# Kernel tuning notes

Measured on AMD Instinct MI355X. Metric: run time of the kernel, lower is better.

Reference implementation:

```python
import jax, jax.numpy as jnp
import numpy as np

H = 8  # num_heads, fixed in the module


def setup_inputs() -> dict:
    key = jax.random.key(0)
    ks = jax.random.split(key, 26)
    C = 256          # hidden_dim
    K = 16           # num_corners
    B = 8            # images
    P = 64           # proposals per image
    N = B * P        # total proposals
    Hf = Wf = 14     # feature map HxW (T = 196 keys per proposal)
    Hq = Wq = 10     # query grid (S = 100 queries)
    s = 1.0 / np.sqrt(C)

    def w(k, shape):
        return jax.random.normal(k, shape, jnp.float32) * s

    return {
        "features": jax.random.normal(ks[0], (N, C, Hf, Wf), jnp.float32),
        "query_features": jax.random.normal(ks[1], (B, C, Hq, Wq), jnp.float32),
        # self-attention params (torch MHA: y = x @ W.T + b)
        "wq_s": w(ks[2], (C, C)), "wk_s": w(ks[3], (C, C)), "wv_s": w(ks[4], (C, C)),
        "bq_s": jnp.zeros((C,), jnp.float32), "bk_s": jnp.zeros((C,), jnp.float32), "bv_s": jnp.zeros((C,), jnp.float32),
        "wo_s": w(ks[5], (C, C)), "bo_s": jnp.zeros((C,), jnp.float32),
        # cross-attention params
        "wq_c": w(ks[6], (C, C)), "wk_c": w(ks[7], (C, C)), "wv_c": w(ks[8], (C, C)),
        "bq_c": jnp.zeros((C,), jnp.float32), "bk_c": jnp.zeros((C,), jnp.float32), "bv_c": jnp.zeros((C,), jnp.float32),
        "wo_c": w(ks[9], (C, C)), "bo_c": jnp.zeros((C,), jnp.float32),
        # polygon MLP head
        "w1": w(ks[10], (C, C)), "b1": jnp.zeros((C,), jnp.float32),
        "w2": w(ks[11], (2 * K, C)), "b2": jnp.zeros((2 * K,), jnp.float32),
        # score head
        "ws": w(ks[12], (1, C)), "bs": jnp.zeros((1,), jnp.float32),
    }


def _forward(features, query_features,
             wq_s, wk_s, wv_s, bq_s, bk_s, bv_s, wo_s, bo_s,
             wq_c, wk_c, wv_c, bq_c, bk_c, bv_c, wo_c, bo_c,
             w1, b1, w2, b2, ws, bs):
    B, C = query_features.shape[0], query_features.shape[1]
    dh = C // H
    scale = 1.0 / jnp.sqrt(jnp.asarray(dh, jnp.float32))

    # query_features: (B,C,Hq,Wq) -> (S,B,C)
    qf = query_features.reshape(B, C, -1).transpose(2, 0, 1)
    S = qf.shape[0]

    # ---- self-attention over queries ----
    q = (qf @ wq_s.T + bq_s).reshape(S, B, H, dh)
    k = (qf @ wk_s.T + bk_s).reshape(S, B, H, dh)
    v = (qf @ wv_s.T + bv_s).reshape(S, B, H, dh)
    att = jax.nn.softmax(jnp.einsum('sbhd,tbhd->bhst', q, k) * scale, axis=-1)
    qsa = jnp.einsum('bhst,tbhd->sbhd', att, v).reshape(S, B, C) @ wo_s.T + bo_s  # (S,B,C)

    # features: (N,C,Hf,Wf) -> (B,P,T,C) with T=Hf*Wf, P=N//B
    N = features.shape[0]
    P = N // B
    feats = features.reshape(N, C, -1).transpose(0, 2, 1).reshape(B, P, -1, C)

    # ---- cross-attention: same (S,C) query broadcast over P proposals ----
    qc = (qsa @ wq_c.T + bq_c).reshape(S, B, H, dh)
    kc = (feats @ wk_c.T + bk_c).reshape(B, P, -1, H, dh)
    vc = (feats @ wv_c.T + bv_c).reshape(B, P, -1, H, dh)
    sc = jnp.einsum('sbhd,bpthd->bphst', qc, kc) * scale  # (B,P,H,S,T)
    a = jax.nn.softmax(sc, axis=-1)
    o = jnp.einsum('bphst,bpthd->bpshd', a, vc).reshape(B, P, S, C) @ wo_c.T + bo_c  # (B,P,S,C)

    # ---- heads, then mean over the S query positions ----
    h1 = jax.nn.relu(o @ w1.T + b1)
    polygons = (h1 @ w2.T + b2).mean(axis=2).reshape(N, -1)          # (N, 2K)
    scores = jax.nn.sigmoid(o @ ws.T + bs).mean(axis=2).reshape(N, 1)  # (N, 1)
    return polygons, scores


def reference(features, query_features,
              wq_s, wk_s, wv_s, bq_s, bk_s, bv_s, wo_s, bo_s,
              wq_c, wk_c, wv_c, bq_c, bk_c, bv_c, wo_c, bo_c,
              w1, b1, w2, b2, ws, bs):
    return _forward(features, query_features,
                    wq_s, wk_s, wv_s, bq_s, bk_s, bv_s, wo_s, bo_s,
                    wq_c, wk_c, wv_c, bq_c, bk_c, bv_c, wo_c, bo_c,
                    w1, b1, w2, b2, ws, bs)
```

## Files before the change

kernel.cpp:

```cpp
#include <hip/hip_runtime.h>
#include <hip/hip_bf16.h>


typedef __attribute__((ext_vector_type(8))) short bf16x8;
typedef __attribute__((ext_vector_type(4))) float f32x4;

__device__ __forceinline__ float bf2f(ushort u) {
    union { float f; uint u32; } v; v.u32 = ((uint)u) << 16; return v.f;
}
__device__ __forceinline__ ushort f2bf(float f) {
    union { float f; uint u; } v; v.f = f;
    uint r = v.u + 0x7FFF + ((v.u >> 16) & 1);
    return (ushort)(r >> 16);
}
__device__ __forceinline__ uint pk2(float a, float b) {
    __hip_bfloat162 h = __float22bfloat162_rn(make_float2(a, b));
    union { __hip_bfloat162 h2; uint u; } c; c.h2 = h; return c.u;
}
__device__ __forceinline__ f32x4 MFMA(bf16x8 a, bf16x8 b, f32x4 c) {
    return __builtin_amdgcn_mfma_f32_16x16x32_bf16(a, b, c, 0, 0, 0);
}

#define SCALE_DH 0.17677669529663687f

#define TOTALW (2337 * 256)
#define QCPN   (8 * 8 * 112 * 32)
#define NBIAS  2337

__global__ void prep_kernel(const float* w0, const float* w1_, const float* w2_,
                            const float* w3, const float* w4, const float* w5,
                            const float* w6, const float* w7, const float* w8,
                            const float* w9, const float* w10,
                            const float* b0, const float* b1_, const float* b2_,
                            const float* b3, const float* b4, const float* b5,
                            const float* b6, const float* b7, const float* b8,
                            const float* b9, const float* b10,
                            ushort* wbf, float* bias, ushort* qcp)
{
    for (size_t i = blockIdx.x * blockDim.x + threadIdx.x;
         i < (size_t)TOTALW + QCPN + NBIAS; i += (size_t)gridDim.x * blockDim.x) {
        if (i < TOTALW) {
            int row = (int)(i >> 8), col = (int)(i & 255);
            const float* sp; int base;
            if      (row < 256)  { sp = w0;  base = 0; }
            else if (row < 512)  { sp = w1_; base = 256; }
            else if (row < 768)  { sp = w2_; base = 512; }
            else if (row < 1024) { sp = w3;  base = 768; }
            else if (row < 1280) { sp = w4;  base = 1024; }
            else if (row < 1536) { sp = w5;  base = 1280; }
            else if (row < 1792) { sp = w6;  base = 1536; }
            else if (row < 2048) { sp = w7;  base = 1792; }
            else if (row < 2304) { sp = w8;  base = 2048; }
            else if (row < 2336) { sp = w9;  base = 2304; }
            else                 { sp = w10; base = 2336; }
            wbf[i] = f2bf(sp[(size_t)(row - base) * 256 + col]);
        } else if (i < (size_t)TOTALW + QCPN) {
            qcp[i - TOTALW] = 0;
        } else {
            int idx = (int)(i - TOTALW - QCPN);
            const float* sp; int base;
            if      (idx < 256)  { sp = b0;  base = 0; }
            else if (idx < 512)  { sp = b1_; base = 256; }
            else if (idx < 768)  { sp = b2_; base = 512; }
            else if (idx < 1024) { sp = b3;  base = 768; }
            else if (idx < 1280) { sp = b4;  base = 1024; }
            else if (idx < 1536) { sp = b5;  base = 1280; }
            else if (idx < 1792) { sp = b6;  base = 1536; }
            else if (idx < 2048) { sp = b7;  base = 1792; }
            else if (idx < 2304) { sp = b8;  base = 2048; }
            else if (idx < 2336) { sp = b9;  base = 2304; }
            else                 { sp = b10; base = 2336; }
            bias[idx] = sp[idx - base];
        }
    }
}

template<int ASRC, int GS, int EPI>
__global__ __launch_bounds__(256)
void gemm_rows(const void* Aptr, const ushort* Wall, const float* Ball,
               ushort* Out, int M, int Wrow0, int Brow0, int ldo)
{
    __shared__ ushort As[64 * 40];
    __shared__ ushort Bs[128 * 40];
    int tid = threadIdx.x;
    int lane = tid & 63, w = tid >> 6;
    int lr = lane & 15, lg = lane >> 4;
    int r0 = blockIdx.x * 64;
    int j0 = blockIdx.y * 128;

    f32x4 acc[4][2];
    #pragma unroll
    for (int mt = 0; mt < 4; ++mt)
        #pragma unroll
        for (int nt = 0; nt < 2; ++nt) { f32x4 z = {0.f,0.f,0.f,0.f}; acc[mt][nt] = z; }

    for (int ks = 0; ks < 8; ++ks) {
        int c0 = ks * 32;
        {
            int i = tid >> 2, q = tid & 3;
            int r = r0 + i;
            if (ASRC == 0) {
                uint4 v = make_uint4(0u,0u,0u,0u);
                if (r < M) v = *(const uint4*)((const ushort*)Aptr + (size_t)r * 256 + c0 + q * 8);
                *(uint4*)(&As[i * 40 + q * 8]) = v;
            } else {
                uint u[4] = {0u,0u,0u,0u};
                if (r < M) {
                    int g = r / GS, o = r - g * GS;
                    const float* src = (const float*)Aptr + (size_t)g * 256 * GS + o;
                    #pragma unroll
                    for (int k2 = 0; k2 < 4; ++k2) {
                        ushort a0 = f2bf(src[(size_t)(c0 + q * 8 + 2 * k2)     * GS]);
                        ushort a1 = f2bf(src[(size_t)(c0 + q * 8 + 2 * k2 + 1) * GS]);
                        u[k2] = (uint)a0 | ((uint)a1 << 16);
                    }
                }
                *(uint4*)(&As[i * 40 + q * 8]) = make_uint4(u[0], u[1], u[2], u[3]);
            }
        }
        {
            int jj = tid >> 1, half = tid & 1;
            const ushort* src = Wall + (size_t)(Wrow0 + j0 + jj) * 256 + c0 + half * 16;
            ushort* dst = &Bs[jj * 40 + half * 16];
            *(uint4*)(dst)     = *(const uint4*)(src);
            *(uint4*)(dst + 8) = *(const uint4*)(src + 8);
        }
        __syncthreads();
        bf16x8 bfr[2];
        #pragma unroll
        for (int nt = 0; nt < 2; ++nt)
            bfr[nt] = *(const bf16x8*)(&Bs[(w * 32 + nt * 16 + lr) * 40 + lg * 8]);
        #pragma unroll
        for (int mt = 0; mt < 4; ++mt) {
            bf16x8 afr = *(const bf16x8*)(&As[(mt * 16 + lr) * 40 + lg * 8]);
            acc[mt][0] = MFMA(afr, bfr[0], acc[mt][0]);
            acc[mt][1] = MFMA(afr, bfr[1], acc[mt][1]);
        }
        __syncthreads();
    }
    #pragma unroll
    for (int mt = 0; mt < 4; ++mt) {
        #pragma unroll
        for (int nt = 0; nt < 2; ++nt) {
            int jc = j0 + w * 32 + nt * 16 + lr;
            float bias = Ball[Brow0 + jc];
            #pragma unroll
            for (int rg = 0; rg < 4; ++rg) {
                int r = r0 + mt * 16 + lg * 4 + rg;
                if (r >= M) continue;
                float vv = acc[mt][nt][rg] + bias;
                if (EPI == 0) {
                    Out[(size_t)r * ldo + jc] = f2bf(vv);
                } else {
                    int b = r / 100, s = r - b * 100;
                    int h = jc >> 5, d = jc & 31;
                    Out[(((size_t)(b * 8 + h)) * 112 + s) * 32 + d] = f2bf(vv * SCALE_DH);
                }
            }
        }
    }
}

__global__ __launch_bounds__(128)
void self_attn(const ushort* qkv, ushort* sav)
{
    __shared__ float kls[100][33];
    __shared__ float vls[100][33];
    __shared__ float sls[100][101];
    int bh = blockIdx.x; int b = bh >> 3, h = bh & 7;
    int tid = threadIdx.x;
    for (int idx = tid; idx < 100 * 32; idx += 128) {
        int t = idx >> 5, d = idx & 31;
        kls[t][d] = bf2f(qkv[((size_t)(b * 100 + t)) * 768 + 256 + h * 32 + d]);
        vls[t][d] = bf2f(qkv[((size_t)(b * 100 + t)) * 768 + 512 + h * 32 + d]);
    }
    __syncthreads();
    if (tid < 100) {
        int s = tid;
        float q[32];
        #pragma unroll
        for (int d = 0; d < 32; ++d)
            q[d] = bf2f(qkv[((size_t)(b * 100 + s)) * 768 + h * 32 + d]) * SCALE_DH;
        float mx = -1e30f;
        for (int t = 0; t < 100; ++t) {
            float sc = 0.f;
            #pragma unroll
            for (int d = 0; d < 32; ++d) sc += q[d] * kls[t][d];
            sls[s][t] = sc; mx = fmaxf(mx, sc);
        }
        float sum = 0.f;
        for (int t = 0; t < 100; ++t) {
            float p = __expf(sls[s][t] - mx);
            sls[s][t] = p; sum += p;
        }
        float inv = 1.f / sum;
        float acc2[32];
        #pragma unroll
        for (int d = 0; d < 32; ++d) acc2[d] = 0.f;
        for (int t = 0; t < 100; ++t) {
            float pv = sls[s][t];
            #pragma unroll
            for (int d = 0; d < 32; ++d) acc2[d] += pv * vls[t][d];
        }
        #pragma unroll
        for (int d = 0; d < 32; ++d)
            sav[((size_t)(b * 100 + s)) * 256 + h * 32 + d] = f2bf(acc2[d] * inv);
    }
}

__global__ __launch_bounds__(512, 2)
void kvproj(const float* features, const ushort* Wall, const float* Ball,
            ushort* kc, ushort* vc, int n_base)
{
    __shared__ ushort featT[224 * 264];
    int tid = threadIdx.x;
    int lane = tid & 63, w = tid >> 6;
    int lr = lane & 15, lg = lane >> 4;
    int nl = blockIdx.x;
    int n  = n_base + nl;
    const float* fb = features + (size_t)n * 256 * 196;

    bf16x8 af[4][8];
    #pragma unroll
    for (int m = 0; m < 4; ++m) {
        int row = ((m < 2) ? 1280 : 1536) + w * 32 + (m & 1) * 16 + lr;
        #pragma unroll
        for (int ks = 0; ks < 8; ++ks)
            af[m][ks] = *(const bf16x8*)(Wall + (size_t)row * 256 + ks * 32 + lg * 8);
    }
    float biask0 = Ball[1280 + w * 32 + lr];
    float biask1 = Ball[1296 + w * 32 + lr];
    float biasv0 = Ball[1536 + w * 32 + lr];
    float biasv1 = Ball[1552 + w * 32 + lr];

    #pragma unroll
    for (int it = 0; it < 7; ++it) {
        int idx = tid + it * 512;
        if (idx < 3136) {
            int cg = idx / 49, tq = idx - cg * 49;
            const float* p = fb + (size_t)(cg * 4) * 196 + tq * 4;
            float4 v0 = *(const float4*)(p);
            float4 v1 = *(const float4*)(p + 196);
            float4 v2 = *(const float4*)(p + 392);
            float4 v3 = *(const float4*)(p + 588);
            #pragma unroll
            for (int j = 0; j < 4; ++j) {
                float e0 = (j == 0) ? v0.x : (j == 1) ? v0.y : (j == 2) ? v0.z : v0.w;
                float e1 = (j == 0) ? v1.x : (j == 1) ? v1.y : (j == 2) ? v1.z : v1.w;
                float e2 = (j == 0) ? v2.x : (j == 1) ? v2.y : (j == 2) ? v2.z : v2.w;
                float e3 = (j == 0) ? v3.x : (j == 1) ? v3.y : (j == 2) ? v3.z : v3.w;
                uint2 pr;
                pr.x = pk2(e0, e1);
                pr.y = pk2(e2, e3);
                *(uint2*)(&featT[(tq * 4 + j) * 264 + cg * 4]) = pr;
            }
        }
    }
    for (int idx = tid; idx < 12 * 264; idx += 512)
        featT[196 * 264 + idx] = 0;
    __syncthreads();

    for (int tt = 0; tt < 13; ++tt) {
        bf16x8 a8[8];
        #pragma unroll
        for (int ks = 0; ks < 8; ++ks)
            a8[ks] = *(const bf16x8*)(&featT[(tt * 16 + lr) * 264 + ks * 32 + lg * 8]);
        f32x4 acc[4];
        #pragma unroll
        for (int m = 0; m < 4; ++m) { f32x4 z = {0.f,0.f,0.f,0.f}; acc[m] = z; }
        #pragma unroll
        for (int ks = 0; ks < 8; ++ks)
            #pragma unroll
            for (int m = 0; m < 4; ++m)
                acc[m] = MFMA(a8[ks], af[m][ks], acc[m]);

        int tb = tt * 16 + lg * 4;
        #pragma unroll
        for (int rg = 0; rg < 4; ++rg) {
            int t = tb + rg;
            if (t < 196) {
                kc[((size_t)nl * 224 + t) * 256 + w * 32 + lr]      = f2bf(acc[0][rg] + biask0);
                kc[((size_t)nl * 224 + t) * 256 + w * 32 + 16 + lr] = f2bf(acc[1][rg] + biask1);
            }
        }
        if (tb < 196) {
            size_t vb0 = ((size_t)nl * 256 + w * 32 + lr) * 224 + tb;
            size_t vb1 = ((size_t)nl * 256 + w * 32 + 16 + lr) * 224 + tb;
            uint a01 = pk2(acc[2][0] + biasv0, acc[2][1] + biasv0);
            uint a23 = pk2(acc[2][2] + biasv0, acc[2][3] + biasv0);
            uint b01 = pk2(acc[3][0] + biasv1, acc[3][1] + biasv1);
            uint b23 = pk2(acc[3][2] + biasv1, acc[3][3] + biasv1);
            *(uint*)(vc + vb0)     = a01;
            *(uint*)(vc + vb0 + 2) = a23;
            *(uint*)(vc + vb1)     = b01;
            *(uint*)(vc + vb1 + 2) = b23;
        }
    }
}

__global__ __launch_bounds__(512, 4)
void attn_fuse(const ushort* qcp, const ushort* kc, const ushort* vc,
               const ushort* Wall, const float* Ball, float* outp, int n_base)
{
    __shared__ char smem[60928];
    ushort* OB  = (ushort*)smem;
    float* hbar = (float*)(smem + 59392);
    float* scb  = (float*)(smem + 60416);

    int tid = threadIdx.x;
    int lane = tid & 63; int w = tid >> 6;
    int lr = lane & 15, lg = lane >> 4;
    int nl = blockIdx.x; int n = n_base + nl;
    int b = n >> 6;
    const ushort* kcn = kc + (size_t)nl * 224 * 256;
    const ushort* vcn = vc + (size_t)nl * 256 * 224;

    bf16x8 qf[7];
    #pragma unroll
    for (int mt = 0; mt < 7; ++mt)
        qf[mt] = *(const bf16x8*)(qcp + ((((size_t)(b * 8 + w)) * 112 + mt * 16 + lr) * 32 + lg * 8));

    bf16x8 ones;
    #pragma unroll
    for (int j = 0; j < 8; ++j) ones[j] = (short)0x3F80;

    f32x4 o_acc[7][2], l_acc[7];
    #pragma unroll
    for (int mt = 0; mt < 7; ++mt) {
        f32x4 z = {0.f,0.f,0.f,0.f};
        o_acc[mt][0] = z; o_acc[mt][1] = z; l_acc[mt] = z;
    }

    const ushort* kbase = kcn + (size_t)lr * 256 + w * 32 + lg * 8;
    const ushort* vb0 = vcn + ((size_t)(w * 32 + lr)) * 224;
    const ushort* vb1 = vcn + ((size_t)(w * 32 + 16 + lr)) * 224;

    bf16x8 ck0, ck1;
    uint2 v0lo, v0hi, v1lo, v1hi;
    ck0 = *(const bf16x8*)(kbase);
    ck1 = *(const bf16x8*)(kbase + 16 * 256);
    v0lo = *(const uint2*)(vb0 + 4 * lg);
    v0hi = *(const uint2*)(vb0 + 16 + 4 * lg);
    v1lo = *(const uint2*)(vb1 + 4 * lg);
    v1hi = *(const uint2*)(vb1 + 16 + 4 * lg);

    for (int ch = 0; ch < 7; ++ch) {
        int t0 = ch * 32;
        bf16x8 nk0, nk1;
        uint2 n0lo, n0hi, n1lo, n1hi;
        if (ch < 6) {
            int t0n = t0 + 32;
            nk0 = *(const bf16x8*)(kbase + (size_t)t0n * 256);
            nk1 = *(const bf16x8*)(kbase + (size_t)(t0n + 16) * 256);
            n0lo = *(const uint2*)(vb0 + t0n + 4 * lg);
            n0hi = *(const uint2*)(vb0 + t0n + 16 + 4 * lg);
            n1lo = *(const uint2*)(vb1 + t0n + 4 * lg);
            n1hi = *(const uint2*)(vb1 + t0n + 16 + 4 * lg);
            if (t0n == 192) {
                uint2 zz = make_uint2(0u, 0u);
                n0hi = zz; n1hi = zz;
                if (lg) { n0lo = zz; n1lo = zz; }
            }
        }
        union { uint4 q; bf16x8 v; } u0, u1;
        u0.q = make_uint4(v0lo.x, v0lo.y, v0hi.x, v0hi.y);
        u1.q = make_uint4(v1lo.x, v1lo.y, v1hi.x, v1hi.y);
        bool mA[4], mB[4];
        #pragma unroll
        for (int r = 0; r < 4; ++r) {
            mA[r] = (t0 + 4 * lg + r)      >= 196;
            mB[r] = (t0 + 16 + 4 * lg + r) >= 196;
        }
        #pragma unroll
        for (int mt = 0; mt < 7; ++mt) {
            f32x4 z = {0.f,0.f,0.f,0.f};
            f32x4 s0 = MFMA(ck0, qf[mt], z);
            f32x4 s1 = MFMA(ck1, qf[mt], z);
            float p00 = mA[0] ? 0.f : __expf(s0[0]);
            float p01 = mA[1] ? 0.f : __expf(s0[1]);
            float p02 = mA[2] ? 0.f : __expf(s0[2]);
            float p03 = mA[3] ? 0.f : __expf(s0[3]);
            float p10 = mB[0] ? 0.f : __expf(s1[0]);
            float p11 = mB[1] ? 0.f : __expf(s1[1]);
            float p12 = mB[2] ? 0.f : __expf(s1[2]);
            float p13 = mB[3] ? 0.f : __expf(s1[3]);
            union { uint4 q; bf16x8 v; } pu;
            pu.q.x = pk2(p00, p01);
            pu.q.y = pk2(p02, p03);
            pu.q.z = pk2(p10, p11);
            pu.q.w = pk2(p12, p13);
            o_acc[mt][0] = MFMA(pu.v, u0.v, o_acc[mt][0]);
            o_acc[mt][1] = MFMA(pu.v, u1.v, o_acc[mt][1]);
            l_acc[mt]    = MFMA(pu.v, ones, l_acc[mt]);
        }
        ck0 = nk0; ck1 = nk1;
        v0lo = n0lo; v0hi = n0hi; v1lo = n1lo; v1hi = n1hi;
    }

    #pragma unroll
    for (int mt = 0; mt < 7; ++mt) {
        #pragma unroll
        for (int r = 0; r < 4; ++r) {
            float inv = 1.f / l_acc[mt][r];
            int srow = mt * 16 + lg * 4 + r;
            OB[srow * 264 + w * 32 + lr]      = f2bf(o_acc[mt][0][r] * inv);
            OB[srow * 264 + w * 32 + 16 + lr] = f2bf(o_acc[mt][1][r] * inv);
        }
    }
    __syncthreads();

    f32x4 a2[7][2];
    #pragma unroll
    for (int mt = 0; mt < 7; ++mt) {
        f32x4 z = {0.f,0.f,0.f,0.f}; a2[mt][0] = z; a2[mt][1] = z;
    }
    for (int ks = 0; ks < 8; ++ks) {
        int c0 = ks * 32;
        bf16x8 bw0 = *(const bf16x8*)(Wall + (size_t)(1792 + w * 32 + lr) * 256 + c0 + lg * 8);
        bf16x8 bw1 = *(const bf16x8*)(Wall + (size_t)(1792 + w * 32 + 16 + lr) * 256 + c0 + lg * 8);
        #pragma unroll
        for (int mt = 0; mt < 7; ++mt) {
            bf16x8 afr = *(const bf16x8*)(&OB[(mt * 16 + lr) * 264 + c0 + lg * 8]);
            a2[mt][0] = MFMA(afr, bw0, a2[mt][0]);
            a2[mt][1] = MFMA(afr, bw1, a2[mt][1]);
        }
    }
    __syncthreads();

    {
        float biasA = Ball[1792 + w * 32 + lr];
        float biasB = Ball[1792 + w * 32 + 16 + lr];
        #pragma unroll
        for (int mt = 0; mt < 7; ++mt)
            #pragma unroll
            for (int r = 0; r < 4; ++r) {
                int srow = mt * 16 + lg * 4 + r;
                OB[srow * 264 + w * 32 + lr]      = f2bf(a2[mt][0][r] + biasA);
                OB[srow * 264 + w * 32 + 16 + lr] = f2bf(a2[mt][1][r] + biasB);
            }
    }
    __syncthreads();

    #pragma unroll
    for (int mt = 0; mt < 7; ++mt) {
        f32x4 z = {0.f,0.f,0.f,0.f}; a2[mt][0] = z; a2[mt][1] = z;
    }
    for (int ks = 0; ks < 8; ++ks) {
        int c0 = ks * 32;
        bf16x8 bw0 = *(const bf16x8*)(Wall + (size_t)(2048 + w * 32 + lr) * 256 + c0 + lg * 8);
        bf16x8 bw1 = *(const bf16x8*)(Wall + (size_t)(2048 + w * 32 + 16 + lr) * 256 + c0 + lg * 8);
        #pragma unroll
        for (int mt = 0; mt < 7; ++mt) {
            bf16x8 afr = *(const bf16x8*)(&OB[(mt * 16 + lr) * 264 + c0 + lg * 8]);
            a2[mt][0] = MFMA(afr, bw0, a2[mt][0]);
            a2[mt][1] = MFMA(afr, bw1, a2[mt][1]);
        }
    }
    if (tid < 100) {
        float s = 0.f;
        for (int c2 = 0; c2 < 256; ++c2)
            s += bf2f(OB[tid * 264 + c2]) * bf2f(Wall[(size_t)2336 * 256 + c2]);
        s += Ball[2336];
        scb[tid] = 1.f / (1.f + __expf(-s));
    }
    __syncthreads();

    {
        float biasA = Ball[2048 + w * 32 + lr];
        float biasB = Ball[2048 + w * 32 + 16 + lr];
        #pragma unroll
        for (int mt = 0; mt < 7; ++mt)
            #pragma unroll
            for (int r = 0; r < 4; ++r) {
                int srow = mt * 16 + lg * 4 + r;
                float vA = a2[mt][0][r] + biasA;
                float vB = a2[mt][1][r] + biasB;
                vA = vA > 0.f ? vA : 0.f;
                vB = vB > 0.f ? vB : 0.f;
                OB[srow * 264 + w * 32 + lr]      = f2bf(vA);
                OB[srow * 264 + w * 32 + 16 + lr] = f2bf(vB);
            }
    }
    __syncthreads();

    if (tid < 256) {
        float s = 0.f;
        for (int srow = 0; srow < 100; ++srow) s += bf2f(OB[srow * 264 + tid]);
        hbar[tid] = s * 0.01f;
    }
    __syncthreads();
    if (tid < 32) {
        float s = 0.f;
        for (int c2 = 0; c2 < 256; ++c2)
            s += hbar[c2] * bf2f(Wall[(size_t)(2304 + tid) * 256 + c2]);
        s += Ball[2304 + tid];
        outp[(size_t)n * 32 + tid] = s;
    }
    if (tid == 64) {
        float s = 0.f;
        for (int i2 = 0; i2 < 100; ++i2) s += scb[i2];
        outp[16384 + n] = s * 0.01f;
    }
}

extern "C" void kernel_launch(void* const* d_in, const int* in_sizes, int n_in,
                              void* d_out, int out_size, void* d_ws, size_t ws_size,
                              hipStream_t stream)
{
    const float* features = (const float*)d_in[0];
    const float* qfeat    = (const float*)d_in[1];
    char* ws = (char*)d_ws;

    ushort* wbf  = (ushort*)ws;
    float*  bias = (float*)(ws + 1196544);
    ushort* qkv  = (ushort*)(ws + 1206016);
    ushort* sav  = (ushort*)(ws + 2434816);
    ushort* osb  = (ushort*)(ws + 2844416);
    ushort* qcp  = (ushort*)(ws + 3254016);
    ushort* kvb  = (ushort*)(ws + 3712768);

    prep_kernel<<<dim3(512), dim3(256), 0, stream>>>(
        (const float*)d_in[2], (const float*)d_in[3], (const float*)d_in[4],
        (const float*)d_in[8], (const float*)d_in[10], (const float*)d_in[11],
        (const float*)d_in[12], (const float*)d_in[16], (const float*)d_in[18],
        (const float*)d_in[20], (const float*)d_in[22],
        (const float*)d_in[5], (const float*)d_in[6], (const float*)d_in[7],
        (const float*)d_in[9], (const float*)d_in[13], (const float*)d_in[14],
        (const float*)d_in[15], (const float*)d_in[17], (const float*)d_in[19],
        (const float*)d_in[21], (const float*)d_in[23],
        wbf, bias, qcp);

    gemm_rows<1, 100, 0><<<dim3(13, 6), dim3(256), 0, stream>>>(
        qfeat, wbf, bias, qkv, 800, 0, 0, 768);
    self_attn<<<dim3(64), dim3(128), 0, stream>>>(qkv, sav);
    gemm_rows<0, 1, 0><<<dim3(13, 2), dim3(256), 0, stream>>>(
        sav, wbf, bias, osb, 800, 768, 768, 256);
    gemm_rows<0, 1, 1><<<dim3(13, 2), dim3(256), 0, stream>>>(
        osb, wbf, bias, qcp, 800, 1024, 1024, 0);

    const size_t per_n = 229376;
    long avail = (long)ws_size - 3712768L;
    int Np = 512;
    if (avail < (long)(per_n * 512)) {
        Np = (int)(avail / (long)per_n);
        if (Np < 1) Np = 1;
    }
    ushort* kcb = kvb;
    ushort* vcb = kvb + (size_t)Np * 224 * 256;
    float* outp = (float*)d_out;
    for (int n0 = 0; n0 < 512; n0 += Np) {
        int cnt = (512 - n0 < Np) ? (512 - n0) : Np;
        kvproj<<<dim3(cnt), dim3(512), 0, stream>>>(features, wbf, bias, kcb, vcb, n0);
        attn_fuse<<<dim3(cnt), dim3(512), 0, stream>>>(qcp, kcb, vcb, wbf, bias, outp, n0);
    }
}
```

Measured before the change: 246.5 us.

## Fold self-attn out-projection into cross Q weights; deepen KV prefetch and split LDS buffers

Adds a kernel that precomputes Wq_c·Wo_s and the combined bias, so one gemm launch over the self-attention output replaces two. In attn_fuse, K/V prefetch goes from one chunk ahead to a three-slot ring two chunks ahead, and s_setprio raises priority around the MFMA loop. A second LDS buffer separates the output-projection result from the ReLU'd MLP activations, letting the score-head dot product run alongside the column mean and removing a barrier. LDS per block grows to about 128 KB and launch bounds drop to 2 blocks per CU, which may cut occupancy; the extra kernel and the rounding of the combined weights to bf16 add some cost and precision change.

```diff
diff --git a/kernel.cpp b/kernel.cpp
--- a/kernel.cpp
+++ b/kernel.cpp
@@ -75,6 +75,25 @@
     }
 }
 
+__global__ __launch_bounds__(256)
+void wcomb(const float* wq_c, const float* wo_s, const float* bq_c,
+           const float* bo_s, ushort* wbf, float* bias)
+{
+    __shared__ float row[256];
+    int i = blockIdx.x, k = threadIdx.x;
+    row[k] = wq_c[(size_t)i * 256 + k];
+    __syncthreads();
+    float acc = 0.f;
+    for (int j = 0; j < 256; ++j)
+        acc = fmaf(row[j], wo_s[(size_t)j * 256 + k], acc);
+    wbf[(size_t)(1024 + i) * 256 + k] = f2bf(acc);
+    if (k == 0) {
+        float s = bq_c[i];
+        for (int j = 0; j < 256; ++j) s += row[j] * bo_s[j];
+        bias[1024 + i] = s;
+    }
+}
+
 template<int ASRC, int GS, int EPI>
 __global__ __launch_bounds__(256)
 void gemm_rows(const void* Aptr, const ushort* Wall, const float* Ball,
@@ -298,14 +317,15 @@
     }
 }
 
-__global__ __launch_bounds__(512, 4)
+__global__ __launch_bounds__(512, 2)
 void attn_fuse(const ushort* qcp, const ushort* kc, const ushort* vc,
                const ushort* Wall, const float* Ball, float* outp, int n_base)
 {
-    __shared__ char smem[60928];
-    ushort* OB  = (ushort*)smem;
+    __shared__ char smem[130816];
+    ushort* OL  = (ushort*)smem;
     float* hbar = (float*)(smem + 59392);
     float* scb  = (float*)(smem + 60416);
+    ushort* O2  = (ushort*)(smem + 71680);
 
     int tid = threadIdx.x;
     int lane = tid & 63; int w = tid >> 6;
@@ -332,50 +352,56 @@
     }
 
     const ushort* kbase = kcn + (size_t)lr * 256 + w * 32 + lg * 8;
-    const ushort* vb0 = vcn + ((size_t)(w * 32 + lr)) * 224;
-    const ushort* vb1 = vcn + ((size_t)(w * 32 + 16 + lr)) * 224;
-
-    bf16x8 ck0, ck1;
-    uint2 v0lo, v0hi, v1lo, v1hi;
-    ck0 = *(const bf16x8*)(kbase);
-    ck1 = *(const bf16x8*)(kbase + 16 * 256);
-    v0lo = *(const uint2*)(vb0 + 4 * lg);
-    v0hi = *(const uint2*)(vb0 + 16 + 4 * lg);
-    v1lo = *(const uint2*)(vb1 + 4 * lg);
-    v1hi = *(const uint2*)(vb1 + 16 + 4 * lg);
-
+    const ushort* vrow0 = vcn + ((size_t)(w * 32 + lr)) * 224;
+    const ushort* vrow1 = vcn + ((size_t)(w * 32 + 16 + lr)) * 224;
+
+    bf16x8 k0[3], k1[3];
+    uint2 va[3], vb[3], vcq[3], vd[3];
+    #pragma unroll
+    for (int pc = 0; pc < 2; ++pc) {
+        int t0n = pc * 32;
+        k0[pc] = *(const bf16x8*)(kbase + (size_t)t0n * 256);
+        k1[pc] = *(const bf16x8*)(kbase + (size_t)(t0n + 16) * 256);
+        va[pc]  = *(const uint2*)(vrow0 + t0n + 4 * lg);
+        vb[pc]  = *(const uint2*)(vrow0 + t0n + 16 + 4 * lg);
+        vcq[pc] = *(const uint2*)(vrow1 + t0n + 4 * lg);
+        vd[pc]  = *(const uint2*)(vrow1 + t0n + 16 + 4 * lg);
+    }
+
+    #pragma unroll
     for (int ch = 0; ch < 7; ++ch) {
+        const int cur = ch % 3;
         int t0 = ch * 32;
-        bf16x8 nk0, nk1;
-        uint2 n0lo, n0hi, n1lo, n1hi;
-        if (ch < 6) {
-            int t0n = t0 + 32;
-            nk0 = *(const bf16x8*)(kbase + (size_t)t0n * 256);
-            nk1 = *(const bf16x8*)(kbase + (size_t)(t0n + 16) * 256);
-            n0lo = *(const uint2*)(vb0 + t0n + 4 * lg);
-            n0hi = *(const uint2*)(vb0 + t0n + 16 + 4 * lg);
-            n1lo = *(const uint2*)(vb1 + t0n + 4 * lg);
-            n1hi = *(const uint2*)(vb1 + t0n + 16 + 4 * lg);
+        if (ch + 2 < 7) {
+            const int nx = (ch + 2) % 3;
+            int t0n = (ch + 2) * 32;
+            k0[nx] = *(const bf16x8*)(kbase + (size_t)t0n * 256);
+            k1[nx] = *(const bf16x8*)(kbase + (size_t)(t0n + 16) * 256);
+            va[nx]  = *(const uint2*)(vrow0 + t0n + 4 * lg);
+            vb[nx]  = *(const uint2*)(vrow0 + t0n + 16 + 4 * lg);
+            vcq[nx] = *(const uint2*)(vrow1 + t0n + 4 * lg);
+            vd[nx]  = *(const uint2*)(vrow1 + t0n + 16 + 4 * lg);
             if (t0n == 192) {
                 uint2 zz = make_uint2(0u, 0u);
-                n0hi = zz; n1hi = zz;
-                if (lg) { n0lo = zz; n1lo = zz; }
+                vb[nx] = zz; vd[nx] = zz;
+                if (lg) { va[nx] = zz; vcq[nx] = zz; }
             }
         }
         union { uint4 q; bf16x8 v; } u0, u1;
-        u0.q = make_uint4(v0lo.x, v0lo.y, v0hi.x, v0hi.y);
-        u1.q = make_uint4(v1lo.x, v1lo.y, v1hi.x, v1hi.y);
+        u0.q = make_uint4(va[cur].x, va[cur].y, vb[cur].x, vb[cur].y);
+        u1.q = make_uint4(vcq[cur].x, vcq[cur].y, vd[cur].x, vd[cur].y);
         bool mA[4], mB[4];
         #pragma unroll
         for (int r = 0; r < 4; ++r) {
             mA[r] = (t0 + 4 * lg + r)      >= 196;
             mB[r] = (t0 + 16 + 4 * lg + r) >= 196;
         }
+        __builtin_amdgcn_s_setprio(1);
         #pragma unroll
         for (int mt = 0; mt < 7; ++mt) {
             f32x4 z = {0.f,0.f,0.f,0.f};
-            f32x4 s0 = MFMA(ck0, qf[mt], z);
-            f32x4 s1 = MFMA(ck1, qf[mt], z);
+            f32x4 s0 = MFMA(k0[cur], qf[mt], z);
+            f32x4 s1 = MFMA(k1[cur], qf[mt], z);
             float p00 = mA[0] ? 0.f : __expf(s0[0]);
             float p01 = mA[1] ? 0.f : __expf(s0[1]);
             float p02 = mA[2] ? 0.f : __expf(s0[2]);
@@ -393,8 +419,7 @@
             o_acc[mt][1] = MFMA(pu.v, u1.v, o_acc[mt][1]);
             l_acc[mt]    = MFMA(pu.v, ones, l_acc[mt]);
         }
-        ck0 = nk0; ck1 = nk1;
-        v0lo = n0lo; v0hi = n0hi; v1lo = n1lo; v1hi = n1hi;
+        __builtin_amdgcn_s_setprio(0);
     }
 
     #pragma unroll
@@ -403,31 +428,29 @@
         for (int r = 0; r < 4; ++r) {
             float inv = 1.f / l_acc[mt][r];
             int srow = mt * 16 + lg * 4 + r;
-            OB[srow * 264 + w * 32 + lr]      = f2bf(o_acc[mt][0][r] * inv);
-            OB[srow * 264 + w * 32 + 16 + lr] = f2bf(o_acc[mt][1][r] * inv);
-        }
-    }
-    __syncthreads();
-
-    f32x4 a2[7][2];
-    #pragma unroll
-    for (int mt = 0; mt < 7; ++mt) {
-        f32x4 z = {0.f,0.f,0.f,0.f}; a2[mt][0] = z; a2[mt][1] = z;
-    }
-    for (int ks = 0; ks < 8; ++ks) {
-        int c0 = ks * 32;
-        bf16x8 bw0 = *(const bf16x8*)(Wall + (size_t)(1792 + w * 32 + lr) * 256 + c0 + lg * 8);
-        bf16x8 bw1 = *(const bf16x8*)(Wall + (size_t)(1792 + w * 32 + 16 + lr) * 256 + c0 + lg * 8);
+            OL[srow * 264 + w * 32 + lr]      = f2bf(o_acc[mt][0][r] * inv);
+            OL[srow * 264 + w * 32 + 16 + lr] = f2bf(o_acc[mt][1][r] * inv);
+        }
+    }
+    __syncthreads();
+
+    {
+        f32x4 a2[7][2];
         #pragma unroll
         for (int mt = 0; mt < 7; ++mt) {
-            bf16x8 afr = *(const bf16x8*)(&OB[(mt * 16 + lr) * 264 + c0 + lg * 8]);
-            a2[mt][0] = MFMA(afr, bw0, a2[mt][0]);
-            a2[mt][1] = MFMA(afr, bw1, a2[mt][1]);
-        }
-    }
-    __syncthreads();
-
-    {
+            f32x4 z = {0.f,0.f,0.f,0.f}; a2[mt][0] = z; a2[mt][1] = z;
+        }
+        for (int ks = 0; ks < 8; ++ks) {
+            int c0 = ks * 32;
+            bf16x8 bw0 = *(const bf16x8*)(Wall + (size_t)(1792 + w * 32 + lr) * 256 + c0 + lg * 8);
+            bf16x8 bw1 = *(const bf16x8*)(Wall + (size_t)(1792 + w * 32 + 16 + lr) * 256 + c0 + lg * 8);
+            #pragma unroll
+            for (int mt = 0; mt < 7; ++mt) {
+                bf16x8 afr = *(const bf16x8*)(&OL[(mt * 16 + lr) * 264 + c0 + lg * 8]);
+                a2[mt][0] = MFMA(afr, bw0, a2[mt][0]);
+                a2[mt][1] = MFMA(afr, bw1, a2[mt][1]);
+            }
+        }
         float biasA = Ball[1792 + w * 32 + lr];
         float biasB = Ball[1792 + w * 32 + 16 + lr];
         #pragma unroll
@@ -435,37 +458,30 @@
             #pragma unroll
             for (int r = 0; r < 4; ++r) {
                 int srow = mt * 16 + lg * 4 + r;
-                OB[srow * 264 + w * 32 + lr]      = f2bf(a2[mt][0][r] + biasA);
-                OB[srow * 264 + w * 32 + 16 + lr] = f2bf(a2[mt][1][r] + biasB);
-            }
-    }
-    __syncthreads();
-
-    #pragma unroll
-    for (int mt = 0; mt < 7; ++mt) {
-        f32x4 z = {0.f,0.f,0.f,0.f}; a2[mt][0] = z; a2[mt][1] = z;
-    }
-    for (int ks = 0; ks < 8; ++ks) {
-        int c0 = ks * 32;
-        bf16x8 bw0 = *(const bf16x8*)(Wall + (size_t)(2048 + w * 32 + lr) * 256 + c0 + lg * 8);
-        bf16x8 bw1 = *(const bf16x8*)(Wall + (size_t)(2048 + w * 32 + 16 + lr) * 256 + c0 + lg * 8);
+                O2[srow * 264 + w * 32 + lr]      = f2bf(a2[mt][0][r] + biasA);
+                O2[srow * 264 + w * 32 + 16 + lr] = f2bf(a2[mt][1][r] + biasB);
+            }
+    }
+    __syncthreads();
+
+    {
+        f32x4 a2[7][2];
         #pragma unroll
         for (int mt = 0; mt < 7; ++mt) {
-            bf16x8 afr = *(const bf16x8*)(&OB[(mt * 16 + lr) * 264 + c0 + lg * 8]);
-            a2[mt][0] = MFMA(afr, bw0, a2[mt][0]);
-            a2[mt][1] = MFMA(afr, bw1, a2[mt][1]);
-        }
-    }
-    if (tid < 100) {
-        float s = 0.f;
-        for (int c2 = 0; c2 < 256; ++c2)
-            s += bf2f(OB[tid * 264 + c2]) * bf2f(Wall[(size_t)2336 * 256 + c2]);
-        s += Ball[2336];
-        scb[tid] = 1.f / (1.f + __expf(-s));
-    }
-    __syncthreads();
-
-    {
+            f32x4 z = {0.f,0.f,0.f,0.f}; a2[mt][0] = z; a2[mt][1] = z;
+        }
+        for (int ks = 0; ks < 8; ++ks) {
+            int c0 = ks * 32;
+            bf16x8 bw0 = *(const bf16x8*)(Wall + (size_t)(2048 + w * 32 + lr) * 256 + c0 + lg * 8);
+            bf16x8 bw1 = *(const bf16x8*)(Wall + (size_t)(2048 + w * 32 + 16 + lr) * 256 + c0 + lg * 8);
+            #pragma unroll
+            for (int mt = 0; mt < 7; ++mt) {
+                bf16x8 afr = *(const bf16x8*)(&O2[(mt * 16 + lr) * 264 + c0 + lg * 8]);
+                a2[mt][0] = MFMA(afr, bw0, a2[mt][0]);
+                a2[mt][1] = MFMA(afr, bw1, a2[mt][1]);
+            }
+        }
+        __syncthreads();
         float biasA = Ball[2048 + w * 32 + lr];
         float biasB = Ball[2048 + w * 32 + 16 + lr];
         #pragma unroll
@@ -477,16 +493,23 @@
                 float vB = a2[mt][1][r] + biasB;
                 vA = vA > 0.f ? vA : 0.f;
                 vB = vB > 0.f ? vB : 0.f;
-                OB[srow * 264 + w * 32 + lr]      = f2bf(vA);
-                OB[srow * 264 + w * 32 + 16 + lr] = f2bf(vB);
+                OL[srow * 264 + w * 32 + lr]      = f2bf(vA);
+                OL[srow * 264 + w * 32 + 16 + lr] = f2bf(vB);
             }
     }
     __syncthreads();
 
     if (tid < 256) {
         float s = 0.f;
-        for (int srow = 0; srow < 100; ++srow) s += bf2f(OB[srow * 264 + tid]);
+        for (int srow = 0; srow < 100; ++srow) s += bf2f(OL[srow * 264 + tid]);
         hbar[tid] = s * 0.01f;
+    }
+    if (tid < 100) {
+        float s = 0.f;
+        for (int c2 = 0; c2 < 256; ++c2)
+            s += bf2f(O2[tid * 264 + c2]) * bf2f(Wall[(size_t)2336 * 256 + c2]);
+        s += Ball[2336];
+        scb[tid] = 1.f / (1.f + __expf(-s));
     }
     __syncthreads();
     if (tid < 32) {
@@ -515,7 +538,6 @@
     float*  bias = (float*)(ws + 1196544);
     ushort* qkv  = (ushort*)(ws + 1206016);
     ushort* sav  = (ushort*)(ws + 2434816);
-    ushort* osb  = (ushort*)(ws + 2844416);
     ushort* qcp  = (ushort*)(ws + 3254016);
     ushort* kvb  = (ushort*)(ws + 3712768);
 
@@ -530,13 +552,15 @@
         (const float*)d_in[21], (const float*)d_in[23],
         wbf, bias, qcp);
 
+    wcomb<<<dim3(256), dim3(256), 0, stream>>>(
+        (const float*)d_in[10], (const float*)d_in[8],
+        (const float*)d_in[13], (const float*)d_in[9], wbf, bias);
+
     gemm_rows<1, 100, 0><<<dim3(13, 6), dim3(256), 0, stream>>>(
         qfeat, wbf, bias, qkv, 800, 0, 0, 768);
     self_attn<<<dim3(64), dim3(128), 0, stream>>>(qkv, sav);
-    gemm_rows<0, 1, 0><<<dim3(13, 2), dim3(256), 0, stream>>>(
-        sav, wbf, bias, osb, 800, 768, 768, 256);
     gemm_rows<0, 1, 1><<<dim3(13, 2), dim3(256), 0, stream>>>(
-        osb, wbf, bias, qcp, 800, 1024, 1024, 0);
+        sav, wbf, bias, qcp, 800, 1024, 1024, 0);
 
     const size_t per_n = 229376;
     long avail = (long)ws_size - 3712768L;
```

Measured after the change: 211.1 us. -14.3%, faster.
